# Performance work log

Measured on AMD Instinct MI355X. Metric: run time of the kernel, lower is better.

Reference implementation:

```python
import jax, jax.numpy as jnp
import numpy as np


def _prelu(x, a):
    return jnp.where(x > 0, x, a * x)


def _conv_row(x, ker, b):
    # torch Conv2d(1,1,(1,3),padding=(0,1)) cross-correlation along width. x: [N,N]
    xp = jnp.pad(x, ((0, 0), (1, 1)))
    return ker[0] * xp[:, :-2] + ker[1] * xp[:, 1:-1] + ker[2] * xp[:, 2:] + b


def _conv_col(x, ker, b):
    # torch Conv2d(1,1,(3,1),padding=(1,0)) cross-correlation along height. x: [N,N]
    xp = jnp.pad(x, ((1, 1), (0, 0)))
    return ker[0] * xp[:-2, :] + ker[1] * xp[1:-1, :] + ker[2] * xp[2:, :] + b


def setup_inputs() -> dict:
    key = jax.random.key(0)
    ks = jax.random.split(key, 16)
    N, D, H, O = 4096, 8, 64, 4
    s = 0.1  # weight scale keeps softmax logits moderate
    f32 = jnp.float32
    inputs = jax.random.normal(ks[0], (1, N, D), f32)
    We = jax.random.normal(ks[1], (D, H), f32) * s
    be = jnp.zeros((H,), f32)
    Wq = jax.random.normal(ks[2], (H, H), f32) * s
    bq = jnp.zeros((H,), f32)
    Wk = jax.random.normal(ks[3], (H, H), f32) * s
    bk = jnp.zeros((H,), f32)
    prelu_a = jnp.array(0.25, f32)
    conv1_k = jax.random.normal(ks[4], (3,), f32) * 0.5
    conv1_b = jnp.array(0.0, f32)
    conv2_k = jax.random.normal(ks[5], (3,), f32) * 0.5
    conv2_b = jnp.array(0.0, f32)
    Wg = jax.random.normal(ks[6], (O, H), f32) * s
    bg = jnp.zeros((H,), f32)
    gcn_a = jnp.array(0.25, f32)
    Wp1 = jax.random.normal(ks[7], (H, H // 2), f32) * s
    bp1 = jnp.zeros((H // 2,), f32)
    Wp2 = jax.random.normal(ks[8], (H // 2, O), f32) * s
    bp2 = jnp.zeros((O,), f32)
    return dict(inputs=inputs, We=We, be=be, Wq=Wq, bq=bq, Wk=Wk, bk=bk,
                prelu_a=prelu_a, conv1_k=conv1_k, conv1_b=conv1_b,
                conv2_k=conv2_k, conv2_b=conv2_b, Wg=Wg, bg=bg, gcn_a=gcn_a,
                Wp1=Wp1, bp1=bp1, Wp2=Wp2, bp2=bp2)


def reference(inputs, We, be, Wq, bq, Wk, bk, prelu_a, conv1_k, conv1_b,
              conv2_k, conv2_b, Wg, bg, gcn_a, Wp1, bp1, Wp2, bp2):
    o = inputs[0, :, :4]                       # [N,4]
    x = inputs[0] @ We + be                    # [N,H]
    q = x @ Wq + bq                            # [N,H]
    k = x @ Wk + bk                            # [N,H]
    scale = 1.0 / jnp.sqrt(jnp.asarray(k.shape[-1], x.dtype))
    scores = jax.nn.softmax((q @ k.T) * scale, axis=-1)  # [N,N]
    cf = scores
    for _ in range(10):  # fixed 10-step stencil loop
        cf = _prelu(_conv_row(cf, conv1_k, conv1_b) + _conv_col(cf, conv2_k, conv2_b), prelu_a)
    mask = (jax.nn.sigmoid(cf) > 0.5).astype(scores.dtype)
    adj = mask * scores                        # adjacency-masked attention [N,N]
    g = _prelu((adj @ o) @ Wg + bg, gcn_a)     # GCN aggregation [N,H]
    pred = jax.nn.relu(g @ Wp1 + bp1) @ Wp2 + bp2  # [N,4]
    return pred[None]                          # [1,N,4]
```

## Files before the change

### kernel.cpp

```cpp
#include <hip/hip_runtime.h>
#include <math.h>

#define NROWS 4096

#define WS_Q    0u
#define WS_K    262144u
#define WS_RS   524288u
#define WS_GPRE 528384u
#define WS_X    544768u
#define BUFC    1048576u
#define BUFE    17825792u
#define WS_NEED 34603008u

static __device__ __forceinline__ float preluf(float x, float a) {
    return x > 0.0f ? x : a * x;
}

__global__ __launch_bounds__(256) void beacon(float* __restrict__ out, float v) {
    int i = blockIdx.x * 256 + threadIdx.x;
    if (i < NROWS * 4) out[i] = v;
}

__global__ __launch_bounds__(256) void zero_rs(float* __restrict__ ws) {
    int i = blockIdx.x * 256 + threadIdx.x;
    if (i < 20480) ws[WS_RS + i] = 0.0f;
}

__global__ __launch_bounds__(256) void embed_x(
    const float* __restrict__ in, const float* __restrict__ We,
    const float* __restrict__ be, float* __restrict__ ws)
{
    int gid = blockIdx.x * 256 + threadIdx.x;
    int i = gid >> 6, h = gid & 63;
    float s = be[h];
    #pragma unroll
    for (int d = 0; d < 8; ++d) s += in[(size_t)i * 8 + d] * We[d * 64 + h];
    ws[WS_X + gid] = s;
}

__global__ __launch_bounds__(256) void qk_proj(
    const float* __restrict__ Wq, const float* __restrict__ bq,
    const float* __restrict__ Wk, const float* __restrict__ bk,
    float* __restrict__ ws)
{
    int gid = blockIdx.x * 256 + threadIdx.x;
    int i = gid >> 6, h = gid & 63;
    const float* x = ws + WS_X + (size_t)i * 64;
    float sq = bq[h], sk = bk[h];
    for (int d = 0; d < 64; ++d) {
        float xv = x[d];
        sq += xv * Wq[d * 64 + h];
        sk += xv * Wk[d * 64 + h];
    }
    ws[WS_Q + gid] = sq;
    ws[WS_K + gid] = sk;
}

__global__ __launch_bounds__(256) void scores_tile(float* __restrict__ ws)
{
    __shared__ float qs[64][68];
    __shared__ float ksT[64][68];
    const int br = blockIdx.y * 64, bc = blockIdx.x * 64;
    const int t = threadIdx.x;

    for (int idx = t; idx < 4096; idx += 256) {
        int r = idx >> 6, d = idx & 63;
        qs[r][d]  = ws[WS_Q + (size_t)(br + r) * 64 + d];
        ksT[d][r] = ws[WS_K + (size_t)(bc + r) * 64 + d];
    }
    __syncthreads();

    const int tr = t >> 4;
    const int tc = t & 15;
    const int r0 = tr * 4, c0 = tc * 4;

    float acc[4][4];
    #pragma unroll
    for (int i = 0; i < 4; ++i)
        #pragma unroll
        for (int j = 0; j < 4; ++j) acc[i][j] = 0.0f;

    #pragma unroll 4
    for (int dd = 0; dd < 64; dd += 4) {
        float4 qv0 = *reinterpret_cast<const float4*>(&qs[r0 + 0][dd]);
        float4 qv1 = *reinterpret_cast<const float4*>(&qs[r0 + 1][dd]);
        float4 qv2 = *reinterpret_cast<const float4*>(&qs[r0 + 2][dd]);
        float4 qv3 = *reinterpret_cast<const float4*>(&qs[r0 + 3][dd]);
        float4 kv0 = *reinterpret_cast<const float4*>(&ksT[dd + 0][c0]);
        float4 kv1 = *reinterpret_cast<const float4*>(&ksT[dd + 1][c0]);
        float4 kv2 = *reinterpret_cast<const float4*>(&ksT[dd + 2][c0]);
        float4 kv3 = *reinterpret_cast<const float4*>(&ksT[dd + 3][c0]);
        #pragma unroll
        for (int i = 0; i < 4; ++i) {
            const float4 qv = (i == 0) ? qv0 : (i == 1) ? qv1 : (i == 2) ? qv2 : qv3;
            acc[i][0] += qv.x * kv0.x; acc[i][1] += qv.x * kv0.y;
            acc[i][2] += qv.x * kv0.z; acc[i][3] += qv.x * kv0.w;
            acc[i][0] += qv.y * kv1.x; acc[i][1] += qv.y * kv1.y;
            acc[i][2] += qv.y * kv1.z; acc[i][3] += qv.y * kv1.w;
            acc[i][0] += qv.z * kv2.x; acc[i][1] += qv.z * kv2.y;
            acc[i][2] += qv.z * kv2.z; acc[i][3] += qv.z * kv2.w;
            acc[i][0] += qv.w * kv3.x; acc[i][1] += qv.w * kv3.y;
            acc[i][2] += qv.w * kv3.z; acc[i][3] += qv.w * kv3.w;
        }
    }

    #pragma unroll
    for (int i = 0; i < 4; ++i) {
        const int r = r0 + i;
        float4 ev;
        ev.x = expf(acc[i][0] * 0.125f);
        ev.y = expf(acc[i][1] * 0.125f);
        ev.z = expf(acc[i][2] * 0.125f);
        ev.w = expf(acc[i][3] * 0.125f);
        float rs = (ev.x + ev.y) + (ev.z + ev.w);
        #pragma unroll
        for (int off = 1; off < 16; off <<= 1) rs += __shfl_xor(rs, off);
        if (tc == 0) atomicAdd(&ws[WS_RS + br + r], rs);
        *reinterpret_cast<float4*>(&ws[BUFE + (size_t)(br + r) * NROWS + bc + c0]) = ev;
    }
}

__global__ __launch_bounds__(256) void stencil_p1(
    const float* __restrict__ c1k, const float* __restrict__ c1b,
    const float* __restrict__ c2k, const float* __restrict__ c2b,
    const float* __restrict__ pa, float* __restrict__ ws)
{
    const int bx = blockIdx.x, by = blockIdx.y;
    const int r0 = by * 64, c0t = bx * 64;
    const int t = threadIdx.x;
    __shared__ float buf[2][74][75];
    __shared__ float il_s[74];

    for (int e = t; e < 74; e += 256) {
        int gr = r0 - 5 + e;
        il_s[e] = ((unsigned)gr < (unsigned)NROWS) ? 1.0f / ws[WS_RS + gr] : 0.0f;
    }
    __syncthreads();

    const bool edge = (bx == 0) || (bx == 63) || (by == 0) || (by == 63);

    {
        const int lci = t % 74;
        const int lr0 = t / 74;
        if (lr0 < 3) {
            if (!edge) {
                const size_t gbase = BUFE + (size_t)(r0 - 5) * NROWS + (c0t - 5) + lci;
                for (int ri = lr0; ri < 74; ri += 3)
                    buf[0][ri][lci] = ws[gbase + (size_t)ri * NROWS] * il_s[ri];
            } else {
                for (int ri = lr0; ri < 74; ri += 3) {
                    int gr = r0 - 5 + ri, gc = c0t - 5 + lci;
                    float v = 0.0f;
                    if ((unsigned)gr < (unsigned)NROWS && (unsigned)gc < (unsigned)NROWS)
                        v = ws[BUFE + (size_t)gr * NROWS + gc] * il_s[ri];
                    buf[0][ri][lci] = v;
                }
            }
        }
    }
    __syncthreads();

    const float k10 = c1k[0], k11 = c1k[1], k12 = c1k[2];
    const float k20 = c2k[0], k21 = c2k[1], k22 = c2k[2];
    const float bb = c1b[0] + c2b[0];
    const float a = pa[0];

    int cur = 0;
    if (!edge) {
        const int ci = 1 + t % 75;
        const int g  = t / 75;
        for (int it = 1; it <= 5; ++it) {
            const int nxt = cur ^ 1;
            if (g < 3 && ci >= it && ci <= 73 - it) {
                const int nr = 74 - 2 * it;
                const int rlo = it + (nr * g) / 3;
                const int rhi = it + (nr * (g + 1)) / 3 - 1;
                float u  = buf[cur][rlo - 1][ci];
                float l  = buf[cur][rlo][ci - 1];
                float c  = buf[cur][rlo][ci];
                float rr = buf[cur][rlo][ci + 1];
                for (int r = rlo; r <= rhi; ++r) {
                    float d = buf[cur][r + 1][ci];
                    float s = k10 * l + k11 * c + k12 * rr + bb +
                              k20 * u + k21 * c + k22 * d;
                    buf[nxt][r][ci] = preluf(s, a);
                    u = c;
                    l = buf[cur][r + 1][ci - 1];
                    rr = buf[cur][r + 1][ci + 1];
                    c = d;
                }
            }
            __syncthreads();
            cur = nxt;
        }
    } else {
        for (int it = 1; it <= 5; ++it) {
            const int nxt = cur ^ 1;
            for (int e = t; e < 72 * 72; e += 256) {
                int ri = 1 + e / 72;
                int ci = 1 + (e - (e / 72) * 72);
                float c_ = buf[cur][ri][ci];
                float lf = buf[cur][ri][ci - 1];
                float rt = buf[cur][ri][ci + 1];
                float up = buf[cur][ri - 1][ci];
                float dn = buf[cur][ri + 1][ci];
                float s = preluf(k10 * lf + k11 * c_ + k12 * rt + bb +
                                 k20 * up + k21 * c_ + k22 * dn, a);
                int gr = r0 - 5 + ri, gc = c0t - 5 + ci;
                bool inm = ((unsigned)gr < (unsigned)NROWS) && ((unsigned)gc < (unsigned)NROWS);
                buf[nxt][ri][ci] = inm ? s : 0.0f;
            }
            __syncthreads();
            cur = nxt;
        }
    }

    #pragma unroll
    for (int k2 = 0; k2 < 16; ++k2) {
        int e = k2 * 256 + t;
        int r = e >> 6, c = e & 63;
        ws[BUFC + (size_t)(r0 + r) * NROWS + (c0t + c)] = buf[cur][5 + r][5 + c];
    }
}

__global__ __launch_bounds__(256) void stencil_p2(
    const float* __restrict__ c1k, const float* __restrict__ c1b,
    const float* __restrict__ c2k, const float* __restrict__ c2b,
    const float* __restrict__ pa, float* __restrict__ ws)
{
    const int bx = blockIdx.x, by = blockIdx.y;
    const int r0 = by * 64, c0t = bx * 64;
    const int t = threadIdx.x;
    __shared__ float buf[2][74][75];
    __shared__ float il_s[74];

    for (int e = t; e < 74; e += 256) {
        int gr = r0 - 5 + e;
        il_s[e] = ((unsigned)gr < (unsigned)NROWS) ? 1.0f / ws[WS_RS + gr] : 0.0f;
    }
    __syncthreads();

    const bool edge = (bx == 0) || (bx == 63) || (by == 0) || (by == 63);

    {
        const int lci = t % 74;
        const int lr0 = t / 74;
        if (lr0 < 3) {
            if (!edge) {
                const size_t gbase = BUFC + (size_t)(r0 - 5) * NROWS + (c0t - 5) + lci;
                for (int ri = lr0; ri < 74; ri += 3)
                    buf[0][ri][lci] = ws[gbase + (size_t)ri * NROWS];
            } else {
                for (int ri = lr0; ri < 74; ri += 3) {
                    int gr = r0 - 5 + ri, gc = c0t - 5 + lci;
                    float v = 0.0f;
                    if ((unsigned)gr < (unsigned)NROWS && (unsigned)gc < (unsigned)NROWS)
                        v = ws[BUFC + (size_t)gr * NROWS + gc];
                    buf[0][ri][lci] = v;
                }
            }
        }
    }
    __syncthreads();

    float sc[16];
    #pragma unroll
    for (int k2 = 0; k2 < 16; ++k2) {
        int e = k2 * 256 + t;
        int r = e >> 6, c = e & 63;
        sc[k2] = ws[BUFE + (size_t)(r0 + r) * NROWS + (c0t + c)] * il_s[5 + r];
    }

    const float k10 = c1k[0], k11 = c1k[1], k12 = c1k[2];
    const float k20 = c2k[0], k21 = c2k[1], k22 = c2k[2];
    const float bb = c1b[0] + c2b[0];
    const float a = pa[0];

    int cur = 0;
    if (!edge) {
        const int ci = 1 + t % 75;
        const int g  = t / 75;
        for (int it = 1; it <= 5; ++it) {
            const int nxt = cur ^ 1;
            if (g < 3 && ci >= it && ci <= 73 - it) {
                const int nr = 74 - 2 * it;
                const int rlo = it + (nr * g) / 3;
                const int rhi = it + (nr * (g + 1)) / 3 - 1;
                float u  = buf[cur][rlo - 1][ci];
                float l  = buf[cur][rlo][ci - 1];
                float c  = buf[cur][rlo][ci];
                float rr = buf[cur][rlo][ci + 1];
                for (int r = rlo; r <= rhi; ++r) {
                    float d = buf[cur][r + 1][ci];
                    float s = k10 * l + k11 * c + k12 * rr + bb +
                              k20 * u + k21 * c + k22 * d;
                    buf[nxt][r][ci] = preluf(s, a);
                    u = c;
                    l = buf[cur][r + 1][ci - 1];
                    rr = buf[cur][r + 1][ci + 1];
                    c = d;
                }
            }
            __syncthreads();
            cur = nxt;
        }
    } else {
        for (int it = 1; it <= 5; ++it) {
            const int nxt = cur ^ 1;
            for (int e = t; e < 72 * 72; e += 256) {
                int ri = 1 + e / 72;
                int ci = 1 + (e - (e / 72) * 72);
                float c_ = buf[cur][ri][ci];
                float lf = buf[cur][ri][ci - 1];
                float rt = buf[cur][ri][ci + 1];
                float up = buf[cur][ri - 1][ci];
                float dn = buf[cur][ri + 1][ci];
                float s = preluf(k10 * lf + k11 * c_ + k12 * rt + bb +
                                 k20 * up + k21 * c_ + k22 * dn, a);
                int gr = r0 - 5 + ri, gc = c0t - 5 + ci;
                bool inm = ((unsigned)gr < (unsigned)NROWS) && ((unsigned)gc < (unsigned)NROWS);
                buf[nxt][ri][ci] = inm ? s : 0.0f;
            }
            __syncthreads();
            cur = nxt;
        }
    }

    #pragma unroll
    for (int k2 = 0; k2 < 16; ++k2) {
        int e = k2 * 256 + t;
        int r = e >> 6, c = e & 63;
        float cf = buf[cur][5 + r][5 + c];
        float ex = expf(-cf);
        float sg = 1.0f / (1.0f + ex);
        float me = (sg > 0.5f) ? sc[k2] : 0.0f;
        ws[BUFE + (size_t)(r0 + r) * NROWS + (c0t + c)] = me;
    }
}

__global__ __launch_bounds__(256) void adj_me(
    const float* __restrict__ in, float* __restrict__ ws)
{
    const int br = blockIdx.y * 64;
    const int jb = blockIdx.x * 256;
    const int t = threadIdx.x;
    __shared__ float os[64][5];
    const int rg = t >> 6, j = t & 63;

    float a0[16], a1[16], a2[16], a3[16];
    #pragma unroll
    for (int rr = 0; rr < 16; ++rr) { a0[rr]=0.f; a1[rr]=0.f; a2[rr]=0.f; a3[rr]=0.f; }

    for (int ch = 0; ch < 4; ++ch) {
        const int c0 = jb + ch * 64;
        __syncthreads();
        { int jj = t >> 2, c = t & 3; os[jj][c] = in[(size_t)(c0 + jj) * 8 + c]; }
        __syncthreads();
        const int rbase = br + rg * 16;
        #pragma unroll
        for (int rr = 0; rr < 16; ++rr) {
            float me = ws[BUFE + (size_t)(rbase + rr) * NROWS + c0 + j];
            a0[rr] += me * os[j][0];
            a1[rr] += me * os[j][1];
            a2[rr] += me * os[j][2];
            a3[rr] += me * os[j][3];
        }
    }
    #pragma unroll
    for (int rr = 0; rr < 16; ++rr) {
        float v0 = a0[rr], v1 = a1[rr], v2 = a2[rr], v3 = a3[rr];
        #pragma unroll
        for (int off = 1; off < 64; off <<= 1) {
            v0 += __shfl_xor(v0, off);
            v1 += __shfl_xor(v1, off);
            v2 += __shfl_xor(v2, off);
            v3 += __shfl_xor(v3, off);
        }
        if (j == 0) {
            const int row = br + rg * 16 + rr;
            atomicAdd(&ws[WS_GPRE + (size_t)row * 4 + 0], v0);
            atomicAdd(&ws[WS_GPRE + (size_t)row * 4 + 1], v1);
            atomicAdd(&ws[WS_GPRE + (size_t)row * 4 + 2], v2);
            atomicAdd(&ws[WS_GPRE + (size_t)row * 4 + 3], v3);
        }
    }
}

__global__ __launch_bounds__(256) void head(
    const float* __restrict__ ws,
    const float* __restrict__ Wg, const float* __restrict__ bg, const float* __restrict__ ga,
    const float* __restrict__ Wp1, const float* __restrict__ bp1,
    const float* __restrict__ Wp2, const float* __restrict__ bp2,
    float* __restrict__ out)
{
    int i = blockIdx.x * 256 + threadIdx.x;
    if (i >= NROWS) return;
    const float a = ga[0];
    float gp[4];
    #pragma unroll
    for (int c = 0; c < 4; ++c) gp[c] = ws[WS_GPRE + (size_t)i * 4 + c];
    float p1[32];
    #pragma unroll
    for (int m = 0; m < 32; ++m) p1[m] = bp1[m];
    for (int h = 0; h < 64; ++h) {
        float s = bg[h];
        #pragma unroll
        for (int c = 0; c < 4; ++c) s += gp[c] * Wg[c * 64 + h];
        float gh = preluf(s, a);
        #pragma unroll
        for (int m = 0; m < 32; ++m) p1[m] += gh * Wp1[h * 32 + m];
    }
    float s0 = bp2[0], s1 = bp2[1], s2 = bp2[2], s3 = bp2[3];
    #pragma unroll
    for (int m = 0; m < 32; ++m) {
        float pm = fmaxf(p1[m], 0.0f);
        s0 += pm * Wp2[m * 4 + 0];
        s1 += pm * Wp2[m * 4 + 1];
        s2 += pm * Wp2[m * 4 + 2];
        s3 += pm * Wp2[m * 4 + 3];
    }
    float4 ov; ov.x = s0; ov.y = s1; ov.z = s2; ov.w = s3;
    *reinterpret_cast<float4*>(out + (size_t)i * 4) = ov;
}

__global__ __launch_bounds__(256) void audit(
    const float* __restrict__ ws, float* __restrict__ out)
{
    __shared__ float red[256];
    const int t = threadIdx.x;
    float mx = 0.0f;
    for (int i = t; i < NROWS * 4; i += 256) {
        float v = ws[WS_GPRE + i];
        if (v != v) mx = 1e30f;
        else mx = fmaxf(mx, fabsf(v));
    }
    red[t] = mx;
    __syncthreads();
    for (int s = 128; s > 0; s >>= 1) {
        if (t < s) red[t] = fmaxf(red[t], red[t + s]);
        __syncthreads();
    }
    const float g = red[0];
    float V = 0.0f;
    if (g >= 1e29f)      V = ldexpf(1.0f, 38);
    else if (g <= 1e-8f) V = ldexpf(1.0f, 36);
    if (V != 0.0f) {
        for (int i = t; i < NROWS * 4; i += 256) out[i] = V;
    }
}

extern "C" void kernel_launch(void* const* d_in, const int* in_sizes, int n_in,
                              void* d_out, int out_size, void* d_ws, size_t ws_size,
                              hipStream_t stream) {
    float* out = (float*)d_out;
    float* ws  = (float*)d_ws;

    static const int dict_sizes[19] = {32768, 512, 64, 4096, 64, 4096, 64,
                                       1, 3, 1, 3, 1, 256, 64, 1, 2048, 32, 128, 4};
    if (n_in != 19) {
        beacon<<<64, 256, 0, stream>>>(out, ldexpf(1.0f + (float)n_in / 256.0f, 40));
        return;
    }
    bool is_dict = true;
    for (int i = 0; i < 19; ++i) if (in_sizes[i] != dict_sizes[i]) is_dict = false;
    if (!is_dict) {
        beacon<<<64, 256, 0, stream>>>(out, ldexpf(1.0f, 42));
        return;
    }
    if (out_size != NROWS * 4) {
        beacon<<<64, 256, 0, stream>>>(out, ldexpf(1.0f, 44));
        return;
    }
    if (ws_size < (size_t)WS_NEED * sizeof(float)) {
        beacon<<<64, 256, 0, stream>>>(out, ldexpf(1.0f, 46));
        return;
    }

    const float* in   = (const float*)d_in[0];
    const float* We   = (const float*)d_in[1];
    const float* be   = (const float*)d_in[2];
    const float* Wq   = (const float*)d_in[3];
    const float* bq   = (const float*)d_in[4];
    const float* Wk   = (const float*)d_in[5];
    const float* bk   = (const float*)d_in[6];
    const float* pa   = (const float*)d_in[7];
    const float* c1k  = (const float*)d_in[8];
    const float* c1b  = (const float*)d_in[9];
    const float* c2k  = (const float*)d_in[10];
    const float* c2b  = (const float*)d_in[11];
    const float* Wg   = (const float*)d_in[12];
    const float* bg   = (const float*)d_in[13];
    const float* ga   = (const float*)d_in[14];
    const float* Wp1  = (const float*)d_in[15];
    const float* bp1  = (const float*)d_in[16];
    const float* Wp2  = (const float*)d_in[17];
    const float* bp2  = (const float*)d_in[18];

    zero_rs<<<80, 256, 0, stream>>>(ws);
    embed_x<<<1024, 256, 0, stream>>>(in, We, be, ws);
    qk_proj<<<1024, 256, 0, stream>>>(Wq, bq, Wk, bk, ws);

    dim3 gt(64, 64);
    scores_tile<<<gt, 256, 0, stream>>>(ws);
    stencil_p1<<<gt, 256, 0, stream>>>(c1k, c1b, c2k, c2b, pa, ws);
    stencil_p2<<<gt, 256, 0, stream>>>(c1k, c1b, c2k, c2b, pa, ws);

    dim3 ga2(16, 64);
    adj_me<<<ga2, 256, 0, stream>>>(in, ws);
    head<<<16, 256, 0, stream>>>(ws, Wg, bg, ga, Wp1, bp1, Wp2, bp2, out);
    audit<<<1, 256, 0, stream>>>(ws, out);
}
```

Before: 373.5 us.

## Fuse adjacency-times-o reduction into stencil pass two and use 32-row stencil tiles

The separate adj_me kernel is removed. Its masked-score times o product and per-row reduction now run at the end of stencil_p2 through wave shuffles and atomics, so the masked N×N matrix is no longer written to global memory and read back. The stencil tiles shrink from 64×64 to 32×64 with a matching halo, which doubles the block count and lowers shared memory per block. In exchange, the halo overhead per tile rises, so more redundant stencil work and more halo loads are done, and there are more atomics per row (one set per 64-column tile rather than per 256-column chunk).

```diff
diff --git a/kernel.cpp b/kernel.cpp
--- a/kernel.cpp
+++ b/kernel.cpp
@@ -2,6 +2,11 @@
 #include <math.h>
 
 #define NROWS 4096
+#define TR 32
+#define TC 64
+#define BR 42
+#define BC 74
+#define BP 75
 
 #define WS_Q    0u
 #define WS_K    262144u
@@ -126,29 +131,29 @@
     const float* __restrict__ pa, float* __restrict__ ws)
 {
     const int bx = blockIdx.x, by = blockIdx.y;
-    const int r0 = by * 64, c0t = bx * 64;
+    const int r0 = by * TR, c0t = bx * TC;
     const int t = threadIdx.x;
-    __shared__ float buf[2][74][75];
-    __shared__ float il_s[74];
-
-    for (int e = t; e < 74; e += 256) {
+    __shared__ float buf[2][BR][BP];
+    __shared__ float il_s[BR];
+
+    for (int e = t; e < BR; e += 256) {
         int gr = r0 - 5 + e;
         il_s[e] = ((unsigned)gr < (unsigned)NROWS) ? 1.0f / ws[WS_RS + gr] : 0.0f;
     }
     __syncthreads();
 
-    const bool edge = (bx == 0) || (bx == 63) || (by == 0) || (by == 63);
+    const bool edge = (bx == 0) || (bx == 63) || (by == 0) || (by == 127);
 
     {
-        const int lci = t % 74;
-        const int lr0 = t / 74;
+        const int lci = t % BC;
+        const int lr0 = t / BC;
         if (lr0 < 3) {
             if (!edge) {
                 const size_t gbase = BUFE + (size_t)(r0 - 5) * NROWS + (c0t - 5) + lci;
-                for (int ri = lr0; ri < 74; ri += 3)
+                for (int ri = lr0; ri < BR; ri += 3)
                     buf[0][ri][lci] = ws[gbase + (size_t)ri * NROWS] * il_s[ri];
             } else {
-                for (int ri = lr0; ri < 74; ri += 3) {
+                for (int ri = lr0; ri < BR; ri += 3) {
                     int gr = r0 - 5 + ri, gc = c0t - 5 + lci;
                     float v = 0.0f;
                     if ((unsigned)gr < (unsigned)NROWS && (unsigned)gc < (unsigned)NROWS)
@@ -167,12 +172,12 @@
 
     int cur = 0;
     if (!edge) {
-        const int ci = 1 + t % 75;
-        const int g  = t / 75;
+        const int ci = 1 + t % 73;
+        const int g  = t / 73;
         for (int it = 1; it <= 5; ++it) {
             const int nxt = cur ^ 1;
-            if (g < 3 && ci >= it && ci <= 73 - it) {
-                const int nr = 74 - 2 * it;
+            if (g < 3 && ci >= it && ci <= (BC - 1) - it) {
+                const int nr = BR - 2 * it;
                 const int rlo = it + (nr * g) / 3;
                 const int rhi = it + (nr * (g + 1)) / 3 - 1;
                 float u  = buf[cur][rlo - 1][ci];
@@ -196,9 +201,9 @@
     } else {
         for (int it = 1; it <= 5; ++it) {
             const int nxt = cur ^ 1;
-            for (int e = t; e < 72 * 72; e += 256) {
-                int ri = 1 + e / 72;
-                int ci = 1 + (e - (e / 72) * 72);
+            for (int e = t; e < (BR - 2) * (BC - 2); e += 256) {
+                int ri = 1 + e / (BC - 2);
+                int ci = 1 + (e - (e / (BC - 2)) * (BC - 2));
                 float c_ = buf[cur][ri][ci];
                 float lf = buf[cur][ri][ci - 1];
                 float rt = buf[cur][ri][ci + 1];
@@ -216,7 +221,7 @@
     }
 
     #pragma unroll
-    for (int k2 = 0; k2 < 16; ++k2) {
+    for (int k2 = 0; k2 < (TR * TC) / 256; ++k2) {
         int e = k2 * 256 + t;
         int r = e >> 6, c = e & 63;
         ws[BUFC + (size_t)(r0 + r) * NROWS + (c0t + c)] = buf[cur][5 + r][5 + c];
@@ -224,34 +229,38 @@
 }
 
 __global__ __launch_bounds__(256) void stencil_p2(
+    const float* __restrict__ in,
     const float* __restrict__ c1k, const float* __restrict__ c1b,
     const float* __restrict__ c2k, const float* __restrict__ c2b,
     const float* __restrict__ pa, float* __restrict__ ws)
 {
     const int bx = blockIdx.x, by = blockIdx.y;
-    const int r0 = by * 64, c0t = bx * 64;
+    const int r0 = by * TR, c0t = bx * TC;
     const int t = threadIdx.x;
-    __shared__ float buf[2][74][75];
-    __shared__ float il_s[74];
-
-    for (int e = t; e < 74; e += 256) {
+    __shared__ float buf[2][BR][BP];
+    __shared__ float il_s[BR];
+
+    for (int e = t; e < BR; e += 256) {
         int gr = r0 - 5 + e;
         il_s[e] = ((unsigned)gr < (unsigned)NROWS) ? 1.0f / ws[WS_RS + gr] : 0.0f;
     }
     __syncthreads();
 
-    const bool edge = (bx == 0) || (bx == 63) || (by == 0) || (by == 63);
+    const bool edge = (bx == 0) || (bx == 63) || (by == 0) || (by == 127);
+
+    const int lc = t & 63;
+    const float4 ov = *reinterpret_cast<const float4*>(in + (size_t)(c0t + lc) * 8);
 
     {
-        const int lci = t % 74;
-        const int lr0 = t / 74;
+        const int lci = t % BC;
+        const int lr0 = t / BC;
         if (lr0 < 3) {
             if (!edge) {
                 const size_t gbase = BUFC + (size_t)(r0 - 5) * NROWS + (c0t - 5) + lci;
-                for (int ri = lr0; ri < 74; ri += 3)
+                for (int ri = lr0; ri < BR; ri += 3)
                     buf[0][ri][lci] = ws[gbase + (size_t)ri * NROWS];
             } else {
-                for (int ri = lr0; ri < 74; ri += 3) {
+                for (int ri = lr0; ri < BR; ri += 3) {
                     int gr = r0 - 5 + ri, gc = c0t - 5 + lci;
                     float v = 0.0f;
                     if ((unsigned)gr < (unsigned)NROWS && (unsigned)gc < (unsigned)NROWS)
@@ -263,9 +272,9 @@
     }
     __syncthreads();
 
-    float sc[16];
-    #pragma unroll
-    for (int k2 = 0; k2 < 16; ++k2) {
+    float sc[(TR * TC) / 256];
+    #pragma unroll
+    for (int k2 = 0; k2 < (TR * TC) / 256; ++k2) {
         int e = k2 * 256 + t;
         int r = e >> 6, c = e & 63;
         sc[k2] = ws[BUFE + (size_t)(r0 + r) * NROWS + (c0t + c)] * il_s[5 + r];
@@ -278,12 +287,12 @@
 
     int cur = 0;
     if (!edge) {
-        const int ci = 1 + t % 75;
-        const int g  = t / 75;
+        const int ci = 1 + t % 73;
+        const int g  = t / 73;
         for (int it = 1; it <= 5; ++it) {
             const int nxt = cur ^ 1;
-            if (g < 3 && ci >= it && ci <= 73 - it) {
-                const int nr = 74 - 2 * it;
+            if (g < 3 && ci >= it && ci <= (BC - 1) - it) {
+                const int nr = BR - 2 * it;
                 const int rlo = it + (nr * g) / 3;
                 const int rhi = it + (nr * (g + 1)) / 3 - 1;
                 float u  = buf[cur][rlo - 1][ci];
@@ -307,9 +316,9 @@
     } else {
         for (int it = 1; it <= 5; ++it) {
             const int nxt = cur ^ 1;
-            for (int e = t; e < 72 * 72; e += 256) {
-                int ri = 1 + e / 72;
-                int ci = 1 + (e - (e / 72) * 72);
+            for (int e = t; e < (BR - 2) * (BC - 2); e += 256) {
+                int ri = 1 + e / (BC - 2);
+                int ci = 1 + (e - (e / (BC - 2)) * (BC - 2));
                 float c_ = buf[cur][ri][ci];
                 float lf = buf[cur][ri][ci - 1];
                 float rt = buf[cur][ri][ci + 1];
@@ -327,61 +336,27 @@
     }
 
     #pragma unroll
-    for (int k2 = 0; k2 < 16; ++k2) {
+    for (int k2 = 0; k2 < (TR * TC) / 256; ++k2) {
         int e = k2 * 256 + t;
         int r = e >> 6, c = e & 63;
         float cf = buf[cur][5 + r][5 + c];
         float ex = expf(-cf);
         float sg = 1.0f / (1.0f + ex);
         float me = (sg > 0.5f) ? sc[k2] : 0.0f;
-        ws[BUFE + (size_t)(r0 + r) * NROWS + (c0t + c)] = me;
-    }
-}
-
-__global__ __launch_bounds__(256) void adj_me(
-    const float* __restrict__ in, float* __restrict__ ws)
-{
-    const int br = blockIdx.y * 64;
-    const int jb = blockIdx.x * 256;
-    const int t = threadIdx.x;
-    __shared__ float os[64][5];
-    const int rg = t >> 6, j = t & 63;
-
-    float a0[16], a1[16], a2[16], a3[16];
-    #pragma unroll
-    for (int rr = 0; rr < 16; ++rr) { a0[rr]=0.f; a1[rr]=0.f; a2[rr]=0.f; a3[rr]=0.f; }
-
-    for (int ch = 0; ch < 4; ++ch) {
-        const int c0 = jb + ch * 64;
-        __syncthreads();
-        { int jj = t >> 2, c = t & 3; os[jj][c] = in[(size_t)(c0 + jj) * 8 + c]; }
-        __syncthreads();
-        const int rbase = br + rg * 16;
-        #pragma unroll
-        for (int rr = 0; rr < 16; ++rr) {
-            float me = ws[BUFE + (size_t)(rbase + rr) * NROWS + c0 + j];
-            a0[rr] += me * os[j][0];
-            a1[rr] += me * os[j][1];
-            a2[rr] += me * os[j][2];
-            a3[rr] += me * os[j][3];
-        }
-    }
-    #pragma unroll
-    for (int rr = 0; rr < 16; ++rr) {
-        float v0 = a0[rr], v1 = a1[rr], v2 = a2[rr], v3 = a3[rr];
+        float p0 = me * ov.x, p1 = me * ov.y, p2 = me * ov.z, p3 = me * ov.w;
         #pragma unroll
         for (int off = 1; off < 64; off <<= 1) {
-            v0 += __shfl_xor(v0, off);
-            v1 += __shfl_xor(v1, off);
-            v2 += __shfl_xor(v2, off);
-            v3 += __shfl_xor(v3, off);
-        }
-        if (j == 0) {
-            const int row = br + rg * 16 + rr;
-            atomicAdd(&ws[WS_GPRE + (size_t)row * 4 + 0], v0);
-            atomicAdd(&ws[WS_GPRE + (size_t)row * 4 + 1], v1);
-            atomicAdd(&ws[WS_GPRE + (size_t)row * 4 + 2], v2);
-            atomicAdd(&ws[WS_GPRE + (size_t)row * 4 + 3], v3);
+            p0 += __shfl_xor(p0, off);
+            p1 += __shfl_xor(p1, off);
+            p2 += __shfl_xor(p2, off);
+            p3 += __shfl_xor(p3, off);
+        }
+        if (c == 0) {
+            const int row = r0 + r;
+            atomicAdd(&ws[WS_GPRE + (size_t)row * 4 + 0], p0);
+            atomicAdd(&ws[WS_GPRE + (size_t)row * 4 + 1], p1);
+            atomicAdd(&ws[WS_GPRE + (size_t)row * 4 + 2], p2);
+            atomicAdd(&ws[WS_GPRE + (size_t)row * 4 + 3], p3);
         }
     }
 }
@@ -502,11 +477,11 @@
 
     dim3 gt(64, 64);
     scores_tile<<<gt, 256, 0, stream>>>(ws);
-    stencil_p1<<<gt, 256, 0, stream>>>(c1k, c1b, c2k, c2b, pa, ws);
-    stencil_p2<<<gt, 256, 0, stream>>>(c1k, c1b, c2k, c2b, pa, ws);
-
-    dim3 ga2(16, 64);
-    adj_me<<<ga2, 256, 0, stream>>>(in, ws);
+
+    dim3 gs(64, 128);
+    stencil_p1<<<gs, 256, 0, stream>>>(c1k, c1b, c2k, c2b, pa, ws);
+    stencil_p2<<<gs, 256, 0, stream>>>(in, c1k, c1b, c2k, c2b, pa, ws);
+
     head<<<16, 256, 0, stream>>>(ws, Wg, bg, ga, Wp1, bp1, Wp2, bp2, out);
     audit<<<1, 256, 0, stream>>>(ws, out);
 }
```

New measurement: 509.9 us. 36.5% more time.
